# Kernel tuning notes

Measured on AMD Instinct MI355X. Metric: run time of the kernel, lower is better.

Reference implementation:

```python
import jax, jax.numpy as jnp
import numpy as np
from jax import lax

B, S, D = 32, 1024, 1024
T = 4                       # entity types
NER_DIM = 1 + 4 * T         # O + {B,I,E,S} per type -> 17
RE_DIM = 16
H = 512                     # RE hidden dim (hard-coded in REModule)
P = 10                      # entity_lim (hard-coded)


def _pair_idx(p):
    # product(l, l) with diagonal removed, row-major order (matches REModule.pairs)
    ii, jj = np.meshgrid(np.arange(p), np.arange(p), indexing='ij')
    m = ii.ravel() != jj.ravel()
    return jnp.asarray(ii.ravel()[m]), jnp.asarray(jj.ravel()[m])

I_IDX, J_IDX = _pair_idx(P)


def setup_inputs() -> dict:
    key = jax.random.key(0)
    ks = jax.random.split(key, 10)
    s = 0.02
    Dx = D + NER_DIM
    return dict(
        h=jax.random.normal(ks[0], (B, S, D), jnp.float32),
        W1=jax.random.normal(ks[1], (D, D), jnp.float32) * s, b1=jnp.zeros((D,), jnp.float32),
        W2=jax.random.normal(ks[2], (D, NER_DIM), jnp.float32) * s, b2=jnp.zeros((NER_DIM,), jnp.float32),
        Wh1=jax.random.normal(ks[3], (Dx, H), jnp.float32) * s, bh1=jnp.zeros((H,), jnp.float32),
        Wh2=jax.random.normal(ks[4], (H, H), jnp.float32) * s, bh2=jnp.zeros((H,), jnp.float32),
        Wt1=jax.random.normal(ks[5], (Dx, H), jnp.float32) * s, bt1=jnp.zeros((H,), jnp.float32),
        Wt2=jax.random.normal(ks[6], (H, H), jnp.float32) * s, bt2=jnp.zeros((H,), jnp.float32),
        Wbil=jax.random.normal(ks[7], (RE_DIM, H, H), jnp.float32) * s, bbil=jnp.zeros((RE_DIM,), jnp.float32),
        Wlin=jax.random.normal(ks[8], (RE_DIM, 2 * H), jnp.float32) * s,
    )


def _forward(h, W1, b1, W2, b2, Wh1, bh1, Wh2, bh2, Wt1, bt1, Wt2, bt2, Wbil, bbil, Wlin):
    Bn = h.shape[0]
    # NER head (2-layer MLP, dropout = identity in eval mode)
    ner = jax.nn.relu(h @ W1 + b1) @ W2 + b2                    # [B,S,NER_DIM]
    x = jnp.concatenate([h, jax.nn.softmax(ner, axis=-1)], -1)  # [B,S,D+NER_DIM]
    x, ner_o = x[:, 1:], ner[:, 1:]                             # drop CLS context token
    Sm = x.shape[1]

    # ---- Entity_filter: vectorized BIOES span decode ----
    # label index convention: O=0, B=1+4t, I=2+4t, E=3+4t, S=4+4t
    amax = jnp.argmax(ner_o, axis=-1)                           # [B,Sm]
    t = jnp.arange(T)
    isB = amax[:, None, :] == (1 + 4 * t)[None, :, None]        # [B,T,Sm]
    isE = amax[:, None, :] == (3 + 4 * t)[None, :, None]
    isS = amax[:, None, :] == (4 + 4 * t)[None, :, None]

    js = jnp.arange(Sm, dtype=jnp.int32)
    # next E strictly after j for each (b,t); Sm if none (matches end = seq_len fallback)
    epos = jnp.where(isE, js, jnp.int32(Sm))
    suff = lax.cummin(epos, axis=2, reverse=True)
    nextE = jnp.concatenate([suff[:, :, 1:], jnp.full((Bn, T, 1), Sm, jnp.int32)], axis=2)

    # sequential acceptance: a B at j is accepted iff j > end of previous accepted span
    def step(end, inp):
        bj, ej, j = inp
        acc = bj & (j > end)
        return jnp.where(acc, ej, end), acc
    end0 = jnp.full((Bn, T), -1, jnp.int32)
    _, accB = lax.scan(step, end0, (jnp.moveaxis(isB, 2, 0), jnp.moveaxis(nextE, 2, 0), js))
    accB = jnp.moveaxis(accB, 0, 2)                             # [B,T,Sm]

    # candidate ordering: per type -> S entities then B entities, col order (matches vstack order)
    valid = jnp.stack([isS, accB], axis=2)                      # [B,T,2,Sm]
    posrec = jnp.stack([jnp.broadcast_to(js, isS.shape), nextE], axis=2)  # recorded position
    Nc = T * 2 * Sm
    keys = jnp.where(valid.reshape(Bn, Nc), jnp.arange(Nc, dtype=jnp.int32), jnp.int32(Nc))
    sel = jnp.sort(keys, axis=-1)[:, :P]                        # first entity_lim candidates
    vs = sel < Nc
    idx = jnp.minimum(sel, Nc - 1)
    kind = (idx // Sm) % 2                                       # 0 = S, 1 = B..E span
    j0 = idx % Sm
    p = jnp.take_along_axis(posrec.reshape(Bn, Nc), idx, axis=1)
    e_eff = jnp.where(kind == 0, j0 + 1, p)                     # exclusive end (S -> single token)

    # segment mean x[b, j0:e_eff] via prefix sums
    csum = jnp.concatenate([jnp.zeros_like(x[:, :1]), jnp.cumsum(x, axis=1)], axis=1)  # [B,Sm+1,Dx]
    seg = jnp.take_along_axis(csum, e_eff[:, :, None], 1) - jnp.take_along_axis(csum, j0[:, :, None], 1)
    denom = jnp.maximum(e_eff - j0, 1).astype(x.dtype)[:, :, None]
    ents = jnp.where(vs[:, :, None], seg / denom, 0.0)          # [B,P,Dx] (PAD value 0)
    pos = jnp.where(vs, p + 1, -1)                              # [B,P]   (PAD value -1)

    # ---- RE module ----
    head = jax.nn.relu(ents @ Wh1 + bh1) @ Wh2 + bh2            # [B,P,H]
    tail = jax.nn.relu(ents @ Wt1 + bt1) @ Wt2 + bt2
    hp, tp = head[:, I_IDX], tail[:, J_IDX]                     # [B,P(P-1),H]
    pos_pairs = jnp.stack([pos[:, I_IDX], pos[:, J_IDX]], -1)   # [B,P(P-1),2]
    re = (jnp.einsum('bph,ohk,bpk->bpo', hp, Wbil, tp) + bbil
          + jnp.concatenate([hp, tp], -1) @ Wlin.T)             # [B,P(P-1),RE_DIM]
    return ner_o, pos_pairs, re


def reference(h, W1, b1, W2, b2, Wh1, bh1, Wh2, bh2, Wt1, bt1, Wt2, bt2, Wbil, bbil, Wlin):
    return _forward(h, W1, b1, W2, b2, Wh1, bh1, Wh2, bh2, Wt1, bt1, Wt2, bt2, Wbil, bbil, Wlin)
```

## Files before the change

kernel.cpp:

```cpp
#include <hip/hip_runtime.h>
#include <hip/hip_bf16.h>

#define BB   32
#define SS   1024
#define DD   1024
#define SMM  1023
#define NER  17
#define HH   512
#define DXX  1041
#define PP   10
#define NPAIR 90

typedef __bf16 bf16x8 __attribute__((ext_vector_type(8)));
typedef float f32x4 __attribute__((ext_vector_type(4)));

__device__ inline void split3(float x, unsigned short& s0, unsigned short& s1, unsigned short& s2) {
  __hip_bfloat16 h0 = __float2bfloat16(x);
  float f0 = __bfloat162float(h0);
  float r1 = x - f0;
  __hip_bfloat16 h1 = __float2bfloat16(r1);
  float f1 = __bfloat162float(h1);
  float r2 = r1 - f1;
  __hip_bfloat16 h2 = __float2bfloat16(r2);
  s0 = *reinterpret_cast<unsigned short*>(&h0);
  s1 = *reinterpret_cast<unsigned short*>(&h1);
  s2 = *reinterpret_cast<unsigned short*>(&h2);
}

__global__ __launch_bounds__(256) void k_split_h(const float4* __restrict__ h4,
                                                 ushort4* __restrict__ p0,
                                                 ushort4* __restrict__ p1,
                                                 ushort4* __restrict__ p2) {
  const int idx = blockIdx.x * 256 + threadIdx.x;
  for (int i = idx; i < 8388608; i += 524288) {
    float4 v = h4[i];
    ushort4 a, b, c;
    split3(v.x, a.x, b.x, c.x);
    split3(v.y, a.y, b.y, c.y);
    split3(v.z, a.z, b.z, c.z);
    split3(v.w, a.w, b.w, c.w);
    p0[i] = a; p1[i] = b; p2[i] = c;
  }
}

__global__ __launch_bounds__(256) void k_split_w(const float* __restrict__ W,
                                                 unsigned short* __restrict__ wP) {
  __shared__ float t[32][33];
  const int bk = blockIdx.x * 32, bn = blockIdx.y * 32;
  const int tr = threadIdx.x >> 5, tc = threadIdx.x & 31;
#pragma unroll
  for (int i = 0; i < 4; ++i)
    t[tr + i * 8][tc] = W[(size_t)(bk + tr + i * 8) * 1024 + bn + tc];
  __syncthreads();
#pragma unroll
  for (int i = 0; i < 4; ++i) {
    const int n = bn + tr + i * 8, k = bk + tc;
    unsigned short s0, s1, s2;
    split3(t[tc][tr + i * 8], s0, s1, s2);
    wP[(size_t)n * 1024 + k] = s0;
    wP[1048576 + (size_t)n * 1024 + k] = s1;
    wP[2097152 + (size_t)n * 1024 + k] = s2;
  }
}

__global__ void k_w2t(const float* __restrict__ W2, float* __restrict__ W2T) {
  const int c = blockIdx.x, k = blockIdx.y * 256 + threadIdx.x;
  W2T[c * 1024 + k] = W2[k * 17 + c];
}

__global__ __launch_bounds__(256) void k_gemm1_mfma(const unsigned short* __restrict__ hP,
                                                    const unsigned short* __restrict__ wP,
                                                    const float* __restrict__ bias,
                                                    float* __restrict__ C) {
  __shared__ unsigned short As[128 * 64];
  __shared__ unsigned short Bs[128 * 64];
  const int tid = threadIdx.x;
  const int w = tid >> 6, l = tid & 63;
  const int bid = blockIdx.x;
  const int wid = (bid & 7) * 256 + (bid >> 3);
  const int m0 = (wid >> 3) * 128;
  const int n0 = (wid & 7) * 128;
  const int lo3 = l & 7;
  const int ksw = ((l & 7) ^ ((l >> 3) & 7)) * 8;
  const int rbase = w * 8 + (l >> 3);
  const int wm = w & 1, wn = w >> 1;
  const int trA = wm * 64 + (l & 15);
  const int trB = wn * 64 + (l & 15);
  const int slotbase = l >> 4;
  f32x4 acc[4][4];
#pragma unroll
  for (int i = 0; i < 4; ++i)
#pragma unroll
    for (int j = 0; j < 4; ++j) acc[i][j] = (f32x4){0.f, 0.f, 0.f, 0.f};

  const unsigned saBits = 2u | (1u << 2) | (0u << 4) | (1u << 6) | (0u << 8) | (0u << 10);
  const unsigned sbBits = 0u | (1u << 2) | (2u << 4) | (0u << 6) | (1u << 8) | (0u << 10);

  for (int step = 0; step < 96; ++step) {
    const int s = step >> 4;
    const int k0 = (step & 15) << 6;
    const int pa = (saBits >> (2 * s)) & 3;
    const int pb = (sbBits >> (2 * s)) & 3;
    const unsigned short* Ab = hP + (size_t)pa * 33554432 + k0 + ksw;
    const unsigned short* Bb = wP + (size_t)pb * 1048576 + k0 + ksw;
#pragma unroll
    for (int i = 0; i < 4; ++i) {
      const int row = rbase + i * 32;
      __builtin_amdgcn_global_load_lds(
          (const __attribute__((address_space(1))) void*)(Ab + (size_t)(m0 + row) * 1024),
          (__attribute__((address_space(3))) void*)((char*)As + i * 4096 + w * 1024 + (l & 63) * 16),
          16, 0, 0);
    }
#pragma unroll
    for (int i = 0; i < 4; ++i) {
      const int row = rbase + i * 32;
      __builtin_amdgcn_global_load_lds(
          (const __attribute__((address_space(1))) void*)(Bb + (size_t)(n0 + row) * 1024),
          (__attribute__((address_space(3))) void*)((char*)Bs + i * 4096 + w * 1024 + (l & 63) * 16),
          16, 0, 0);
    }
    __syncthreads();
#pragma unroll
    for (int kk2 = 0; kk2 < 2; ++kk2) {
      bf16x8 af[4], bfr[4];
#pragma unroll
      for (int m = 0; m < 4; ++m) {
        const int row = trA + m * 16;
        const int byte = row * 128 + ((((kk2 << 2) + slotbase) ^ lo3) << 4);
        af[m] = *(const bf16x8*)((const char*)As + byte);
      }
#pragma unroll
      for (int n = 0; n < 4; ++n) {
        const int row = trB + n * 16;
        const int byte = row * 128 + ((((kk2 << 2) + slotbase) ^ lo3) << 4);
        bfr[n] = *(const bf16x8*)((const char*)Bs + byte);
      }
#pragma unroll
      for (int m = 0; m < 4; ++m)
#pragma unroll
        for (int n = 0; n < 4; ++n)
          acc[m][n] = __builtin_amdgcn_mfma_f32_16x16x32_bf16(af[m], bfr[n], acc[m][n], 0, 0, 0);
    }
    __syncthreads();
  }
  const int crow0 = m0 + wm * 64 + (l >> 4) * 4;
  const int ccol0 = n0 + wn * 64 + (l & 15);
#pragma unroll
  for (int n = 0; n < 4; ++n) {
    const int col = ccol0 + n * 16;
    const float bb = bias[col];
#pragma unroll
    for (int m = 0; m < 4; ++m)
#pragma unroll
      for (int r = 0; r < 4; ++r) {
        const int row = crow0 + m * 16 + r;
        C[(size_t)row * 1024 + col] = fmaxf(acc[m][n][r] + bb, 0.f);
      }
  }
}

__global__ __launch_bounds__(256) void k_gemm1(const float* __restrict__ A,
                                               const float* __restrict__ Bm,
                                               const float* __restrict__ bias,
                                               float* __restrict__ C) {
  __shared__ float As[16][128];
  __shared__ float Bsh[16][128];
  const int tid = threadIdx.x;
  const int tx = tid & 15, ty = tid >> 4;
  const int n0 = blockIdx.x * 128, m0 = blockIdx.y * 128;
  const int ar = tid >> 1, ak = (tid & 1) * 8;
  const int bk = tid >> 4, bc = (tid & 15) * 8;
  float acc[2][2][4][4] = {};
  for (int k0 = 0; k0 < 1024; k0 += 16) {
    float4 a0 = *(const float4*)(A + (size_t)(m0 + ar) * 1024 + k0 + ak);
    float4 a1 = *(const float4*)(A + (size_t)(m0 + ar) * 1024 + k0 + ak + 4);
    float4 b0 = *(const float4*)(Bm + (size_t)(k0 + bk) * 1024 + n0 + bc);
    float4 b1v = *(const float4*)(Bm + (size_t)(k0 + bk) * 1024 + n0 + bc + 4);
    __syncthreads();
    As[ak + 0][ar] = a0.x; As[ak + 1][ar] = a0.y; As[ak + 2][ar] = a0.z; As[ak + 3][ar] = a0.w;
    As[ak + 4][ar] = a1.x; As[ak + 5][ar] = a1.y; As[ak + 6][ar] = a1.z; As[ak + 7][ar] = a1.w;
    *(float4*)&Bsh[bk][bc] = b0;
    *(float4*)&Bsh[bk][bc + 4] = b1v;
    __syncthreads();
#pragma unroll
    for (int kk = 0; kk < 16; ++kk) {
      float4 aA = *(const float4*)&As[kk][ty * 4];
      float4 aB = *(const float4*)&As[kk][64 + ty * 4];
      float4 bA = *(const float4*)&Bsh[kk][tx * 4];
      float4 bB = *(const float4*)&Bsh[kk][64 + tx * 4];
      float av[2][4] = {{aA.x, aA.y, aA.z, aA.w}, {aB.x, aB.y, aB.z, aB.w}};
      float bv[2][4] = {{bA.x, bA.y, bA.z, bA.w}, {bB.x, bB.y, bB.z, bB.w}};
#pragma unroll
      for (int ri = 0; ri < 2; ++ri)
#pragma unroll
        for (int i = 0; i < 4; ++i)
#pragma unroll
          for (int rj = 0; rj < 2; ++rj)
#pragma unroll
            for (int j = 0; j < 4; ++j)
              acc[ri][rj][i][j] = fmaf(av[ri][i], bv[rj][j], acc[ri][rj][i][j]);
    }
  }
#pragma unroll
  for (int ri = 0; ri < 2; ++ri)
#pragma unroll
    for (int i = 0; i < 4; ++i) {
      int row = m0 + ri * 64 + ty * 4 + i;
#pragma unroll
      for (int rj = 0; rj < 2; ++rj) {
        int col = n0 + rj * 64 + tx * 4;
        float4 o;
        o.x = fmaxf(acc[ri][rj][i][0] + bias[col + 0], 0.f);
        o.y = fmaxf(acc[ri][rj][i][1] + bias[col + 1], 0.f);
        o.z = fmaxf(acc[ri][rj][i][2] + bias[col + 2], 0.f);
        o.w = fmaxf(acc[ri][rj][i][3] + bias[col + 3], 0.f);
        *(float4*)(C + (size_t)row * 1024 + col) = o;
      }
    }
}

__global__ __launch_bounds__(256) void k_ner(const float* __restrict__ C1,
                                             const float* __restrict__ W2T,
                                             const float* __restrict__ b2,
                                             float* __restrict__ ner_out,
                                             float* __restrict__ softm,
                                             int* __restrict__ amax) {
  const int wave = threadIdx.x >> 6, lane = threadIdx.x & 63;
  const int row0 = blockIdx.x * 16 + wave * 4;
  float acc[4][17];
#pragma unroll
  for (int r = 0; r < 4; ++r)
#pragma unroll
    for (int c = 0; c < 17; ++c) acc[r][c] = 0.f;
  for (int kb = 0; kb < 16; ++kb) {
    int k = kb * 64 + lane;
    float w2l[17];
#pragma unroll
    for (int c = 0; c < 17; ++c) w2l[c] = W2T[c * 1024 + k];
#pragma unroll
    for (int r = 0; r < 4; ++r) {
      float v = C1[(size_t)(row0 + r) * 1024 + k];
#pragma unroll
      for (int c = 0; c < 17; ++c) acc[r][c] = fmaf(v, w2l[c], acc[r][c]);
    }
  }
#pragma unroll
  for (int off = 32; off > 0; off >>= 1) {
#pragma unroll
    for (int r = 0; r < 4; ++r)
#pragma unroll
      for (int c = 0; c < 17; ++c) acc[r][c] += __shfl_xor(acc[r][c], off);
  }
  if (lane < 4) {
    const int row = row0 + lane;
    float v[17];
#pragma unroll
    for (int c = 0; c < 17; ++c) v[c] = acc[lane][c] + b2[c];
    float mx = v[0]; int am = 0;
#pragma unroll
    for (int c = 1; c < 17; ++c) { if (v[c] > mx) { mx = v[c]; am = c; } }
    float s = 0.f, e[17];
#pragma unroll
    for (int c = 0; c < 17; ++c) { e[c] = __expf(v[c] - mx); s += e[c]; }
    const float inv = 1.f / s;
    float* sm = softm + (size_t)row * 17;
#pragma unroll
    for (int c = 0; c < 17; ++c) sm[c] = e[c] * inv;
    amax[row] = am;
    const int b = row >> 10, sidx = row & 1023;
    if (sidx >= 1) {
      float* no = ner_out + ((size_t)b * SMM + sidx - 1) * 17;
#pragma unroll
      for (int c = 0; c < 17; ++c) no[c] = v[c];
    }
  }
}

__global__ __launch_bounds__(64) void k_spans(const int* __restrict__ amax,
                                              int* __restrict__ meta,
                                              float* __restrict__ pp_out) {
  const int b = blockIdx.x, lane = threadIdx.x;
  __shared__ int nextE[4][1023];
  __shared__ int slist[4][10], blj[4][10], ble[4][10];
  __shared__ int ns[4], nb[4];
  __shared__ int posq[10];
  const int* am = amax + b * 1024 + 1;
  if (lane < 4) {
    const int t = lane;
    int cur = SMM;
    for (int j = SMM - 1; j >= 0; --j) {
      nextE[t][j] = cur;
      if (am[j] == 3 + 4 * t) cur = j;
    }
    int end = -1, cs = 0, cb = 0;
    for (int j = 0; j < SMM; ++j) {
      int a = am[j];
      if (a == 4 + 4 * t && cs < 10) slist[t][cs++] = j;
      if (a == 1 + 4 * t && j > end) {
        end = nextE[t][j];
        if (cb < 10) { blj[t][cb] = j; ble[t][cb] = end; cb++; }
      }
    }
    ns[t] = cs; nb[t] = cb;
  }
  __syncthreads();
  if (lane == 0) {
    int q = 0;
    for (int t = 0; t < 4 && q < 10; ++t) {
      for (int s = 0; s < ns[t] && q < 10; ++s) {
        int j = slist[t][s];
        int* m = meta + (b * 10 + q) * 4;
        m[0] = j; m[1] = j + 1; m[2] = 1; m[3] = 1;
        posq[q] = j + 1; ++q;
      }
      for (int s = 0; s < nb[t] && q < 10; ++s) {
        int j = blj[t][s], e = ble[t][s];
        int* m = meta + (b * 10 + q) * 4;
        m[0] = j; m[1] = e; m[2] = e - j; m[3] = 1;
        posq[q] = e + 1; ++q;
      }
    }
    for (; q < 10; ++q) {
      int* m = meta + (b * 10 + q) * 4;
      m[0] = 0; m[1] = 0; m[2] = 1; m[3] = 0;
      posq[q] = -1;
    }
  }
  __syncthreads();
  for (int pr = lane; pr < NPAIR; pr += 64) {
    int i = pr / 9, jj = pr % 9;
    int j = jj + (jj >= i ? 1 : 0);
    pp_out[(size_t)(b * NPAIR + pr) * 2 + 0] = (float)posq[i];
    pp_out[(size_t)(b * NPAIR + pr) * 2 + 1] = (float)posq[j];
  }
}

__global__ __launch_bounds__(256) void k_ents(const float* __restrict__ h,
                                              const float* __restrict__ softm,
                                              const int* __restrict__ meta,
                                              float* __restrict__ ents) {
  const int bq = blockIdx.x;
  const int b = bq / 10;
  const int* m = meta + bq * 4;
  const int j0 = m[0], e = m[1], len = m[2], vs = m[3];
  float acc[5] = {0.f, 0.f, 0.f, 0.f, 0.f};
  for (int row = j0; row < e; ++row) {
    const int s = row + 1;
    const float* hr = h + (size_t)(b * 1024 + s) * 1024;
    const float* sr = softm + (size_t)(b * 1024 + s) * 17;
#pragma unroll
    for (int i = 0; i < 5; ++i) {
      int d = threadIdx.x + i * 256;
      if (d < DXX) acc[i] += (d < 1024 ? hr[d] : sr[d - 1024]);
    }
  }
  const float inv = vs ? (1.0f / (float)len) : 0.0f;
#pragma unroll
  for (int i = 0; i < 5; ++i) {
    int d = threadIdx.x + i * 256;
    if (d < DXX) ents[(size_t)bq * DXX + d] = acc[i] * inv;
  }
}

__global__ __launch_bounds__(512) void k_mlp_l1(const float* __restrict__ ents,
                                                const float* __restrict__ Wh1, const float* __restrict__ bh1,
                                                const float* __restrict__ Wt1, const float* __restrict__ bt1,
                                                float* __restrict__ H1, float* __restrict__ T1) {
  __shared__ float e[2][DXX];
  const int r0 = blockIdx.x * 2;
  const int chain = blockIdx.y;
  const float* W = chain ? Wt1 : Wh1;
  const float* bi = chain ? bt1 : bh1;
  float* out = chain ? T1 : H1;
  for (int idx = threadIdx.x; idx < 2 * DXX; idx += 512) {
    int row = idx >= DXX;
    int col = row ? idx - DXX : idx;
    e[row][col] = ents[(size_t)(r0 + row) * DXX + col];
  }
  __syncthreads();
  const int n = threadIdx.x;
  float a0 = 0.f, a1 = 0.f;
#pragma unroll 4
  for (int k = 0; k < DXX; ++k) {
    float w = W[(size_t)k * 512 + n];
    a0 = fmaf(e[0][k], w, a0);
    a1 = fmaf(e[1][k], w, a1);
  }
  const float bv = bi[n];
  out[(size_t)r0 * 512 + n] = fmaxf(a0 + bv, 0.f);
  out[(size_t)(r0 + 1) * 512 + n] = fmaxf(a1 + bv, 0.f);
}

__global__ __launch_bounds__(512) void k_mlp_l2(const float* __restrict__ H1, const float* __restrict__ T1,
                                                const float* __restrict__ Wh2, const float* __restrict__ bh2,
                                                const float* __restrict__ Wt2, const float* __restrict__ bt2,
                                                float* __restrict__ headp, float* __restrict__ tailp) {
  __shared__ float e[2][512];
  const int r0 = blockIdx.x * 2;
  const int chain = blockIdx.y;
  const float* in = chain ? T1 : H1;
  const float* W = chain ? Wt2 : Wh2;
  const float* bi = chain ? bt2 : bh2;
  float* out = chain ? tailp : headp;
  for (int idx = threadIdx.x; idx < 1024; idx += 512)
    e[idx >> 9][idx & 511] = in[(size_t)r0 * 512 + idx];
  __syncthreads();
  const int n = threadIdx.x;
  float a0 = 0.f, a1 = 0.f;
#pragma unroll 4
  for (int k = 0; k < 512; ++k) {
    float w = W[(size_t)k * 512 + n];
    a0 = fmaf(e[0][k], w, a0);
    a1 = fmaf(e[1][k], w, a1);
  }
  const float bv = bi[n];
  out[(size_t)r0 * 512 + n] = a0 + bv;
  out[(size_t)(r0 + 1) * 512 + n] = a1 + bv;
}

__global__ __launch_bounds__(512) void k_bil(const float* __restrict__ headp,
                                             const float* __restrict__ Wbil,
                                             float* __restrict__ u) {
  __shared__ float hs[16 * 512];
  const int m0 = blockIdx.x * 16;
  const int o = blockIdx.y;
  for (int idx = threadIdx.x; idx < 16 * 512; idx += 512)
    hs[idx] = headp[(size_t)m0 * 512 + idx];
  __syncthreads();
  const int n = threadIdx.x;
  const float* Wo = Wbil + (size_t)o * 262144;
  float acc[16];
#pragma unroll
  for (int i = 0; i < 16; ++i) acc[i] = 0.f;
  for (int k = 0; k < 512; ++k) {
    float w = Wo[(size_t)k * 512 + n];
#pragma unroll
    for (int i = 0; i < 16; ++i) acc[i] = fmaf(hs[i * 512 + k], w, acc[i]);
  }
#pragma unroll
  for (int i = 0; i < 16; ++i)
    u[((size_t)o * 320 + m0 + i) * 512 + n] = acc[i];
}

__global__ __launch_bounds__(256) void k_lin(const float* __restrict__ headp,
                                             const float* __restrict__ tailp,
                                             const float* __restrict__ Wlin,
                                             float* __restrict__ lh,
                                             float* __restrict__ lt) {
  __shared__ float redH[4][16], redT[4][16];
  const int r = blockIdx.x;
  const int wv = threadIdx.x >> 6, lane = threadIdx.x & 63;
  const float* hr = headp + (size_t)r * 512;
  const float* tr = tailp + (size_t)r * 512;
  float a[16], bacc[16];
#pragma unroll
  for (int o = 0; o < 16; ++o) { a[o] = 0.f; bacc[o] = 0.f; }
#pragma unroll
  for (int kk = 0; kk < 2; ++kk) {
    const int k = wv * 128 + kk * 64 + lane;
    const float hv = hr[k], tv = tr[k];
#pragma unroll
    for (int o = 0; o < 16; ++o) {
      a[o] = fmaf(hv, Wlin[o * 1024 + k], a[o]);
      bacc[o] = fmaf(tv, Wlin[o * 1024 + 512 + k], bacc[o]);
    }
  }
#pragma unroll
  for (int off = 32; off > 0; off >>= 1) {
#pragma unroll
    for (int o = 0; o < 16; ++o) {
      a[o] += __shfl_xor(a[o], off);
      bacc[o] += __shfl_xor(bacc[o], off);
    }
  }
  if (lane == 0) {
#pragma unroll
    for (int o = 0; o < 16; ++o) { redH[wv][o] = a[o]; redT[wv][o] = bacc[o]; }
  }
  __syncthreads();
  if (threadIdx.x < 16) {
    const int o = threadIdx.x;
    float s = 0.f, t = 0.f;
#pragma unroll
    for (int w2 = 0; w2 < 4; ++w2) { s += redH[w2][o]; t += redT[w2][o]; }
    lh[r * 16 + o] = s;
    lt[r * 16 + o] = t;
  }
}

__global__ __launch_bounds__(256) void k_re(const float* __restrict__ u,
                                            const float* __restrict__ tailp,
                                            const float* __restrict__ lh,
                                            const float* __restrict__ lt,
                                            const float* __restrict__ bbil,
                                            float* __restrict__ re_out) {
  const int bp = blockIdx.x;
  const int b = bp / NPAIR, pr = bp % NPAIR;
  const int i = pr / 9, jj = pr % 9;
  const int j = jj + (jj >= i ? 1 : 0);
  const int wave = threadIdx.x >> 6, lane = threadIdx.x & 63;
  const float* tj = tailp + (size_t)(b * 10 + j) * 512;
#pragma unroll
  for (int oo = 0; oo < 4; ++oo) {
    const int o = wave + oo * 4;
    const float* uo = u + ((size_t)o * 320 + b * 10 + i) * 512;
    float acc = 0.f;
    for (int k = lane; k < 512; k += 64) acc = fmaf(uo[k], tj[k], acc);
#pragma unroll
    for (int off = 32; off > 0; off >>= 1) acc += __shfl_xor(acc, off);
    if (lane == 0)
      re_out[(size_t)bp * 16 + o] = acc + bbil[o] + lh[(b * 10 + i) * 16 + o] + lt[(b * 10 + j) * 16 + o];
  }
}

extern "C" void kernel_launch(void* const* d_in, const int* in_sizes, int n_in,
                              void* d_out, int out_size, void* d_ws, size_t ws_size,
                              hipStream_t stream) {
  const float* h    = (const float*)d_in[0];
  const float* W1   = (const float*)d_in[1];
  const float* b1   = (const float*)d_in[2];
  const float* W2   = (const float*)d_in[3];
  const float* b2   = (const float*)d_in[4];
  const float* Wh1  = (const float*)d_in[5];
  const float* bh1  = (const float*)d_in[6];
  const float* Wh2  = (const float*)d_in[7];
  const float* bh2  = (const float*)d_in[8];
  const float* Wt1  = (const float*)d_in[9];
  const float* bt1  = (const float*)d_in[10];
  const float* Wt2  = (const float*)d_in[11];
  const float* bt2  = (const float*)d_in[12];
  const float* Wbil = (const float*)d_in[13];
  const float* bbil = (const float*)d_in[14];
  const float* Wlin = (const float*)d_in[15];

  float* out = (float*)d_out;
  float* ner_out = out;
  float* pp_out  = out + 556512;
  float* re_out  = out + 562272;

  char* ws = (char*)d_ws;
  float* C1    = (float*)(ws + 0);
  float* softm = (float*)(ws + 134217728);
  int*   amax  = (int*)  (ws + 136445952);
  int*   meta  = (int*)  (ws + 136577024);
  float* ents  = (float*)(ws + 136582144);
  float* H1    = (float*)(ws + 137914624);
  float* T1    = (float*)(ws + 138569984);
  float* headp = (float*)(ws + 139225344);
  float* tailp = (float*)(ws + 139880704);
  float* u     = (float*)(ws + 140536064);
  float* lh    = (float*)(ws + 151021824);
  float* lt    = (float*)(ws + 151042304);
  float* W2T   = (float*)(ws + 151062784);
  unsigned short* wP = (unsigned short*)(ws + 151132416);
  unsigned short* hP = (unsigned short*)(ws + 157423872);
  const size_t NEED_FULL = 358750464;
  const size_t NEED_W2T  = 151132416;

  const bool full = ws_size >= NEED_FULL;
  const bool haveW2T = ws_size >= NEED_W2T;

  if (full) {
    k_split_h<<<2048, 256, 0, stream>>>((const float4*)h, (ushort4*)hP,
                                        (ushort4*)(hP + 33554432), (ushort4*)(hP + 67108864));
    k_split_w<<<dim3(32, 32), 256, 0, stream>>>(W1, wP);
    k_gemm1_mfma<<<2048, 256, 0, stream>>>(hP, wP, b1, C1);
  } else {
    k_gemm1<<<dim3(8, 256), 256, 0, stream>>>(h, W1, b1, C1);
  }
  if (haveW2T) {
    k_w2t<<<dim3(17, 4), 256, 0, stream>>>(W2, W2T);
    k_ner<<<2048, 256, 0, stream>>>(C1, W2T, b2, ner_out, softm, amax);
  } else {
    k_w2t<<<dim3(17, 4), 256, 0, stream>>>(W2, (float*)(ws + 140536064));
    k_ner<<<2048, 256, 0, stream>>>(C1, (float*)(ws + 140536064), b2, ner_out, softm, amax);
  }
  k_spans<<<32, 64, 0, stream>>>(amax, meta, pp_out);
  k_ents<<<320, 256, 0, stream>>>(h, softm, meta, ents);
  k_mlp_l1<<<dim3(160, 2), 512, 0, stream>>>(ents, Wh1, bh1, Wt1, bt1, H1, T1);
  k_mlp_l2<<<dim3(160, 2), 512, 0, stream>>>(H1, T1, Wh2, bh2, Wt2, bt2, headp, tailp);
  k_bil<<<dim3(20, 16), 512, 0, stream>>>(headp, Wbil, u);
  k_lin<<<320, 256, 0, stream>>>(headp, tailp, Wlin, lh, lt);
  k_re<<<2880, 256, 0, stream>>>(u, tailp, lh, lt, bbil, re_out);
}
```

Before: 1.387 ms.

## Pipeline the split-bf16 GEMM with larger tiles and double-buffered LDS, and retile the bilinear kernel

Replaces the 128x128 single-buffered MFMA GEMM with a 256x256 tile, 512-thread kernel. It double-buffers LDS and interleaves the global-to-LDS loads for the next k-tile with MFMA quads, using explicit vmcnt waits, barriers and raised wave priority. The aim is to hide load latency and raise arithmetic intensity for the dominant GEMM. The bilinear projection kernel is also rewritten as a classic 64x64 register-tiled SGEMM, replacing a per-thread column loop. The cost is higher register and LDS pressure and hand-tuned synchronisation that is fragile to get right.

```diff
diff --git a/kernel.cpp b/kernel.cpp
--- a/kernel.cpp
+++ b/kernel.cpp
@@ -13,6 +13,12 @@
 
 typedef __bf16 bf16x8 __attribute__((ext_vector_type(8)));
 typedef float f32x4 __attribute__((ext_vector_type(4)));
+
+#define VMCNT(n) asm volatile("s_waitcnt vmcnt(" #n ")" ::: "memory")
+#define BAR_MEM() asm volatile("s_barrier" ::: "memory")
+
+#define SA_BITS (2u | (1u << 2) | (0u << 4) | (1u << 6) | (0u << 8) | (0u << 10))
+#define SB_BITS (0u | (1u << 2) | (2u << 4) | (0u << 6) | (1u << 8) | (0u << 10))
 
 __device__ inline void split3(float x, unsigned short& s0, unsigned short& s1, unsigned short& s2) {
   __hip_bfloat16 h0 = __float2bfloat16(x);
@@ -68,94 +74,181 @@
   W2T[c * 1024 + k] = W2[k * 17 + c];
 }
 
-__global__ __launch_bounds__(256) void k_gemm1_mfma(const unsigned short* __restrict__ hP,
-                                                    const unsigned short* __restrict__ wP,
-                                                    const float* __restrict__ bias,
-                                                    float* __restrict__ C) {
-  __shared__ unsigned short As[128 * 64];
-  __shared__ unsigned short Bs[128 * 64];
+__global__ __launch_bounds__(512, 2) void k_gemm1_8ph(const unsigned short* __restrict__ hP,
+                                                      const unsigned short* __restrict__ wP,
+                                                      const float* __restrict__ bias,
+                                                      float* __restrict__ C) {
+  __shared__ unsigned short LA[2][16384];
+  __shared__ unsigned short LB[2][16384];
   const int tid = threadIdx.x;
   const int w = tid >> 6, l = tid & 63;
+  const int wm = w >> 2, wn = w & 3;
   const int bid = blockIdx.x;
-  const int wid = (bid & 7) * 256 + (bid >> 3);
-  const int m0 = (wid >> 3) * 128;
-  const int n0 = (wid & 7) * 128;
-  const int lo3 = l & 7;
-  const int ksw = ((l & 7) ^ ((l >> 3) & 7)) * 8;
-  const int rbase = w * 8 + (l >> 3);
-  const int wm = w & 1, wn = w >> 1;
-  const int trA = wm * 64 + (l & 15);
-  const int trB = wn * 64 + (l & 15);
-  const int slotbase = l >> 4;
-  f32x4 acc[4][4];
-#pragma unroll
-  for (int i = 0; i < 4; ++i)
+  const int wid = (bid & 7) * 64 + (bid >> 3);
+  const int m0 = (wid >> 2) * 256;
+  const int n0 = (wid & 3) * 256;
+  const int srow = tid >> 3;
+  const int sk = ((tid & 7) ^ (srow & 7)) * 8;
+  const int fr = l & 15;
+  const int fslot = l >> 4;
+
+  f32x4 acc[8][4];
+#pragma unroll
+  for (int i = 0; i < 8; ++i)
 #pragma unroll
     for (int j = 0; j < 4; ++j) acc[i][j] = (f32x4){0.f, 0.f, 0.f, 0.f};
 
-  const unsigned saBits = 2u | (1u << 2) | (0u << 4) | (1u << 6) | (0u << 8) | (0u << 10);
-  const unsigned sbBits = 0u | (1u << 2) | (2u << 4) | (0u << 6) | (1u << 8) | (0u << 10);
-
-  for (int step = 0; step < 96; ++step) {
-    const int s = step >> 4;
-    const int k0 = (step & 15) << 6;
-    const int pa = (saBits >> (2 * s)) & 3;
-    const int pb = (sbBits >> (2 * s)) & 3;
-    const unsigned short* Ab = hP + (size_t)pa * 33554432 + k0 + ksw;
-    const unsigned short* Bb = wP + (size_t)pb * 1048576 + k0 + ksw;
-#pragma unroll
-    for (int i = 0; i < 4; ++i) {
-      const int row = rbase + i * 32;
+  auto stage = [&](int buf, int which, int half, int tile) {
+    const int s = tile >> 4, k0 = (tile & 15) << 6;
+    const unsigned short* base;
+    if (which == 0)
+      base = hP + (size_t)((SA_BITS >> (2 * s)) & 3) * 33554432 + (size_t)(m0 + half * 128) * 1024;
+    else
+      base = wP + (size_t)((SB_BITS >> (2 * s)) & 3) * 1048576 + (size_t)(n0 + half * 128) * 1024;
+    char* lds = (char*)(which ? LB[buf] : LA[buf]) + half * 16384;
+#pragma unroll
+    for (int i = 0; i < 2; ++i) {
       __builtin_amdgcn_global_load_lds(
-          (const __attribute__((address_space(1))) void*)(Ab + (size_t)(m0 + row) * 1024),
-          (__attribute__((address_space(3))) void*)((char*)As + i * 4096 + w * 1024 + (l & 63) * 16),
-          16, 0, 0);
-    }
-#pragma unroll
-    for (int i = 0; i < 4; ++i) {
-      const int row = rbase + i * 32;
-      __builtin_amdgcn_global_load_lds(
-          (const __attribute__((address_space(1))) void*)(Bb + (size_t)(n0 + row) * 1024),
-          (__attribute__((address_space(3))) void*)((char*)Bs + i * 4096 + w * 1024 + (l & 63) * 16),
-          16, 0, 0);
-    }
-    __syncthreads();
-#pragma unroll
-    for (int kk2 = 0; kk2 < 2; ++kk2) {
-      bf16x8 af[4], bfr[4];
-#pragma unroll
-      for (int m = 0; m < 4; ++m) {
-        const int row = trA + m * 16;
-        const int byte = row * 128 + ((((kk2 << 2) + slotbase) ^ lo3) << 4);
-        af[m] = *(const bf16x8*)((const char*)As + byte);
-      }
-#pragma unroll
-      for (int n = 0; n < 4; ++n) {
-        const int row = trB + n * 16;
-        const int byte = row * 128 + ((((kk2 << 2) + slotbase) ^ lo3) << 4);
-        bfr[n] = *(const bf16x8*)((const char*)Bs + byte);
-      }
-#pragma unroll
-      for (int m = 0; m < 4; ++m)
-#pragma unroll
-        for (int n = 0; n < 4; ++n)
-          acc[m][n] = __builtin_amdgcn_mfma_f32_16x16x32_bf16(af[m], bfr[n], acc[m][n], 0, 0, 0);
-    }
-    __syncthreads();
-  }
-  const int crow0 = m0 + wm * 64 + (l >> 4) * 4;
-  const int ccol0 = n0 + wn * 64 + (l & 15);
-#pragma unroll
-  for (int n = 0; n < 4; ++n) {
-    const int col = ccol0 + n * 16;
-    const float bb = bias[col];
-#pragma unroll
-    for (int m = 0; m < 4; ++m)
-#pragma unroll
-      for (int r = 0; r < 4; ++r) {
-        const int row = crow0 + m * 16 + r;
-        C[(size_t)row * 1024 + col] = fmaxf(acc[m][n][r] + bb, 0.f);
-      }
+          (const __attribute__((address_space(1))) void*)(base + (size_t)(srow + 64 * i) * 1024 + k0 + sk),
+          (__attribute__((address_space(3))) void*)(lds + i * 8192 + tid * 16), 16, 0, 0);
+    }
+  };
+  auto rdA = [&](int buf, int f, int ks) -> bf16x8 {
+    const int row = (2 * f + wm) * 16 + fr;
+    const int phys = (ks * 4 + fslot) ^ (row & 7);
+    return *(const bf16x8*)((const char*)LA[buf] + row * 128 + phys * 16);
+  };
+  auto rdB = [&](int buf, int nf, int ks) -> bf16x8 {
+    const int row = (4 * wn + nf) * 16 + fr;
+    const int phys = (ks * 4 + fslot) ^ (row & 7);
+    return *(const bf16x8*)((const char*)LB[buf] + row * 128 + phys * 16);
+  };
+
+  stage(0, 0, 0, 0); __builtin_amdgcn_sched_barrier(0);
+  stage(0, 1, 0, 0); __builtin_amdgcn_sched_barrier(0);
+  stage(0, 1, 1, 0); __builtin_amdgcn_sched_barrier(0);
+  stage(0, 0, 1, 0); __builtin_amdgcn_sched_barrier(0);
+  VMCNT(2);
+  BAR_MEM();
+
+#define MFMA_QUAD(q, aq)                                                        \
+  __builtin_amdgcn_s_setprio(1);                                                \
+  _Pragma("unroll") for (int f2 = 0; f2 < 2; ++f2)                              \
+    _Pragma("unroll") for (int nf = 0; nf < 4; ++nf)                            \
+      _Pragma("unroll") for (int ks = 0; ks < 2; ++ks)                          \
+        acc[2 * (q) + f2][nf] = __builtin_amdgcn_mfma_f32_16x16x32_bf16(        \
+            aq[f2][ks], bfrag[nf][ks], acc[2 * (q) + f2][nf], 0, 0, 0);         \
+  __builtin_amdgcn_s_setprio(0);
+
+  for (int t = 0; t < 95; ++t) {
+    const int cb = t & 1, nb = cb ^ 1;
+    bf16x8 bfrag[4][2];
+#pragma unroll
+    for (int nf = 0; nf < 4; ++nf)
+#pragma unroll
+      for (int ks = 0; ks < 2; ++ks) bfrag[nf][ks] = rdB(cb, nf, ks);
+    {
+      bf16x8 aq[2][2];
+#pragma unroll
+      for (int f2 = 0; f2 < 2; ++f2)
+#pragma unroll
+        for (int ks = 0; ks < 2; ++ks) aq[f2][ks] = rdA(cb, f2, ks);
+      stage(nb, 0, 0, t + 1); __builtin_amdgcn_sched_barrier(0);
+      __builtin_amdgcn_s_barrier();
+      MFMA_QUAD(0, aq);
+      BAR_MEM();
+    }
+    {
+      bf16x8 aq[2][2];
+#pragma unroll
+      for (int f2 = 0; f2 < 2; ++f2)
+#pragma unroll
+        for (int ks = 0; ks < 2; ++ks) aq[f2][ks] = rdA(cb, 2 + f2, ks);
+      stage(nb, 1, 0, t + 1); __builtin_amdgcn_sched_barrier(0);
+      __builtin_amdgcn_s_barrier();
+      MFMA_QUAD(1, aq);
+      VMCNT(4);
+      BAR_MEM();
+    }
+    {
+      bf16x8 aq[2][2];
+#pragma unroll
+      for (int f2 = 0; f2 < 2; ++f2)
+#pragma unroll
+        for (int ks = 0; ks < 2; ++ks) aq[f2][ks] = rdA(cb, 4 + f2, ks);
+      stage(nb, 1, 1, t + 1); __builtin_amdgcn_sched_barrier(0);
+      __builtin_amdgcn_s_barrier();
+      MFMA_QUAD(2, aq);
+      BAR_MEM();
+    }
+    {
+      bf16x8 aq[2][2];
+#pragma unroll
+      for (int f2 = 0; f2 < 2; ++f2)
+#pragma unroll
+        for (int ks = 0; ks < 2; ++ks) aq[f2][ks] = rdA(cb, 6 + f2, ks);
+      stage(nb, 0, 1, t + 1); __builtin_amdgcn_sched_barrier(0);
+      __builtin_amdgcn_s_barrier();
+      MFMA_QUAD(3, aq);
+      VMCNT(2);
+      BAR_MEM();
+    }
+  }
+  {
+    const int cb = 1;
+    bf16x8 bfrag[4][2];
+#pragma unroll
+    for (int nf = 0; nf < 4; ++nf)
+#pragma unroll
+      for (int ks = 0; ks < 2; ++ks) bfrag[nf][ks] = rdB(cb, nf, ks);
+    {
+      bf16x8 aq[2][2];
+#pragma unroll
+      for (int f2 = 0; f2 < 2; ++f2)
+#pragma unroll
+        for (int ks = 0; ks < 2; ++ks) aq[f2][ks] = rdA(cb, f2, ks);
+      __builtin_amdgcn_s_barrier();
+      MFMA_QUAD(0, aq);
+    }
+    {
+      bf16x8 aq[2][2];
+#pragma unroll
+      for (int f2 = 0; f2 < 2; ++f2)
+#pragma unroll
+        for (int ks = 0; ks < 2; ++ks) aq[f2][ks] = rdA(cb, 2 + f2, ks);
+      MFMA_QUAD(1, aq);
+      VMCNT(0);
+      BAR_MEM();
+    }
+    {
+      bf16x8 aq[2][2];
+#pragma unroll
+      for (int f2 = 0; f2 < 2; ++f2)
+#pragma unroll
+        for (int ks = 0; ks < 2; ++ks) aq[f2][ks] = rdA(cb, 4 + f2, ks);
+      MFMA_QUAD(2, aq);
+    }
+    {
+      bf16x8 aq[2][2];
+#pragma unroll
+      for (int f2 = 0; f2 < 2; ++f2)
+#pragma unroll
+        for (int ks = 0; ks < 2; ++ks) aq[f2][ks] = rdA(cb, 6 + f2, ks);
+      MFMA_QUAD(3, aq);
+    }
+  }
+#undef MFMA_QUAD
+#pragma unroll
+  for (int f = 0; f < 8; ++f) {
+    const int row0 = m0 + (2 * f + wm) * 16 + (l >> 4) * 4;
+#pragma unroll
+    for (int nf = 0; nf < 4; ++nf) {
+      const int col = n0 + (4 * wn + nf) * 16 + (l & 15);
+      const float bb = bias[col];
+#pragma unroll
+      for (int r = 0; r < 4; ++r)
+        C[(size_t)(row0 + r) * 1024 + col] = fmaxf(acc[f][nf][r] + bb, 0.f);
+    }
   }
 }
 
@@ -418,28 +511,44 @@
   out[(size_t)(r0 + 1) * 512 + n] = a1 + bv;
 }
 
-__global__ __launch_bounds__(512) void k_bil(const float* __restrict__ headp,
+__global__ __launch_bounds__(256) void k_bil(const float* __restrict__ headp,
                                              const float* __restrict__ Wbil,
                                              float* __restrict__ u) {
-  __shared__ float hs[16 * 512];
-  const int m0 = blockIdx.x * 16;
-  const int o = blockIdx.y;
-  for (int idx = threadIdx.x; idx < 16 * 512; idx += 512)
-    hs[idx] = headp[(size_t)m0 * 512 + idx];
-  __syncthreads();
-  const int n = threadIdx.x;
+  __shared__ float As[16][64];
+  __shared__ float Bs[16][64];
+  const int o = blockIdx.z;
+  const int m0 = blockIdx.y * 64, n0 = blockIdx.x * 64;
+  const int tx = threadIdx.x & 15, ty = threadIdx.x >> 4;
   const float* Wo = Wbil + (size_t)o * 262144;
-  float acc[16];
-#pragma unroll
-  for (int i = 0; i < 16; ++i) acc[i] = 0.f;
-  for (int k = 0; k < 512; ++k) {
-    float w = Wo[(size_t)k * 512 + n];
-#pragma unroll
-    for (int i = 0; i < 16; ++i) acc[i] = fmaf(hs[i * 512 + k], w, acc[i]);
-  }
-#pragma unroll
-  for (int i = 0; i < 16; ++i)
-    u[((size_t)o * 320 + m0 + i) * 512 + n] = acc[i];
+  float acc[4][4] = {};
+  for (int k0 = 0; k0 < 512; k0 += 16) {
+    float4 av4 = *(const float4*)(headp + (size_t)(m0 + (threadIdx.x >> 2)) * 512 + k0 + (threadIdx.x & 3) * 4);
+    float4 bv4 = *(const float4*)(Wo + (size_t)(k0 + (threadIdx.x >> 4)) * 512 + n0 + (threadIdx.x & 15) * 4);
+    __syncthreads();
+    As[(threadIdx.x & 3) * 4 + 0][threadIdx.x >> 2] = av4.x;
+    As[(threadIdx.x & 3) * 4 + 1][threadIdx.x >> 2] = av4.y;
+    As[(threadIdx.x & 3) * 4 + 2][threadIdx.x >> 2] = av4.z;
+    As[(threadIdx.x & 3) * 4 + 3][threadIdx.x >> 2] = av4.w;
+    *(float4*)&Bs[threadIdx.x >> 4][(threadIdx.x & 15) * 4] = bv4;
+    __syncthreads();
+#pragma unroll
+    for (int kk = 0; kk < 16; ++kk) {
+      float4 a = *(const float4*)&As[kk][ty * 4];
+      float4 b = *(const float4*)&Bs[kk][tx * 4];
+      float av[4] = {a.x, a.y, a.z, a.w};
+      float bv[4] = {b.x, b.y, b.z, b.w};
+#pragma unroll
+      for (int i = 0; i < 4; ++i)
+#pragma unroll
+        for (int j = 0; j < 4; ++j)
+          acc[i][j] = fmaf(av[i], bv[j], acc[i][j]);
+    }
+  }
+#pragma unroll
+  for (int i = 0; i < 4; ++i) {
+    float4 ov = {acc[i][0], acc[i][1], acc[i][2], acc[i][3]};
+    *(float4*)(u + ((size_t)o * 320 + m0 + ty * 4 + i) * 512 + n0 + tx * 4) = ov;
+  }
 }
 
 __global__ __launch_bounds__(256) void k_lin(const float* __restrict__ headp,
@@ -564,7 +673,7 @@
     k_split_h<<<2048, 256, 0, stream>>>((const float4*)h, (ushort4*)hP,
                                         (ushort4*)(hP + 33554432), (ushort4*)(hP + 67108864));
     k_split_w<<<dim3(32, 32), 256, 0, stream>>>(W1, wP);
-    k_gemm1_mfma<<<2048, 256, 0, stream>>>(hP, wP, b1, C1);
+    k_gemm1_8ph<<<512, 512, 0, stream>>>(hP, wP, b1, C1);
   } else {
     k_gemm1<<<dim3(8, 256), 256, 0, stream>>>(h, W1, b1, C1);
   }
@@ -579,7 +688,7 @@
   k_ents<<<320, 256, 0, stream>>>(h, softm, meta, ents);
   k_mlp_l1<<<dim3(160, 2), 512, 0, stream>>>(ents, Wh1, bh1, Wt1, bt1, H1, T1);
   k_mlp_l2<<<dim3(160, 2), 512, 0, stream>>>(H1, T1, Wh2, bh2, Wt2, bt2, headp, tailp);
-  k_bil<<<dim3(20, 16), 512, 0, stream>>>(headp, Wbil, u);
+  k_bil<<<dim3(8, 5, 16), 256, 0, stream>>>(headp, Wbil, u);
   k_lin<<<320, 256, 0, stream>>>(headp, tailp, Wlin, lh, lt);
   k_re<<<2880, 256, 0, stream>>>(u, tailp, lh, lt, bbil, re_out);
 }
```

New measurement: 1.252 ms. 9.7% less time.
